# Performance work log

Measured on AMD Instinct MI355X. Metric: run time of the kernel, lower is better.

## Reference

```python
import jax, jax.numpy as jnp
import numpy as np
import math

DIM = 512
WINDOW = 4
TOPK = 8


def setup_inputs() -> dict:
    key = jax.random.key(0)
    ks = jax.random.split(key, 14)
    B, N, D = 4, 4096, DIM
    s = 0.02
    return {
        'mu':  jax.random.normal(ks[0], (B, N, D), jnp.float32),
        'Wq':  jax.random.normal(ks[1], (D, D), jnp.float32) * s,
        'bq':  jnp.zeros((D,), jnp.float32),
        'Wk':  jax.random.normal(ks[2], (D, D), jnp.float32) * s,
        'bk':  jnp.zeros((D,), jnp.float32),
        'Wv':  jax.random.normal(ks[3], (D, D), jnp.float32) * s,
        'bv':  jnp.zeros((D,), jnp.float32),
        'Wm1': jax.random.normal(ks[4], (2 * D, D), jnp.float32) * s,
        'bm1': jnp.zeros((D,), jnp.float32),
        'Wm2': jax.random.normal(ks[5], (D, D), jnp.float32) * s,
        'bm2': jnp.zeros((D,), jnp.float32),
        'Wo':  jax.random.normal(ks[6], (2 * D, D), jnp.float32) * s,
        'bo':  jnp.zeros((D,), jnp.float32),
    }


def reference(mu, Wq, bq, Wk, bk, Wv, bv, Wm1, bm1, Wm2, bm2, Wo, bo):
    B, N, D = mu.shape
    W = WINDOW
    # ---- local windowed message passing ----
    padded = jnp.pad(mu, ((0, 0), (W, 0), (0, 0)))  # left-pad seq with W zeros
    # neighbors[:, n, w-1] = mu[:, n-w] (zeros if n-w < 0); [B, N, W, D]
    neighbors = jnp.stack([padded[:, W - w:W - w + N, :] for w in range(1, W + 1)], axis=2)
    self_exp = jnp.broadcast_to(mu[:, :, None, :], neighbors.shape)
    h = jnp.concatenate([self_exp, neighbors], axis=-1)  # [B, N, W, 2D]
    h = jax.nn.silu(h @ Wm1 + bm1)
    local_msgs = (h @ Wm2 + bm2).mean(axis=2)  # [B, N, D]
    # ---- sparse causal global attention ----
    q = mu @ Wq + bq
    k = mu @ Wk + bk
    v = mu @ Wv + bv
    scores = jnp.einsum('bnd,bmd->bnm', q, k) * (1.0 / math.sqrt(D))
    causal = jnp.tril(jnp.ones((N, N), bool))
    scores = jnp.where(causal, scores, -jnp.inf)
    # top-k then softmax over kept entries == softmax over scatter(-inf elsewhere)
    topk_vals, topk_idx = jax.lax.top_k(scores, TOPK)  # [B, N, K]
    probs = jax.nn.softmax(topk_vals, axis=-1)
    bi = jnp.arange(B)[:, None, None]
    ni = jnp.arange(N)[None, :, None]
    attn = jnp.zeros_like(scores).at[bi, ni, topk_idx].set(probs)  # [B, N, N]
    global_msgs = jnp.einsum('bnm,bmd->bnd', attn, v)
    return jnp.concatenate([local_msgs, global_msgs], axis=-1) @ Wo + bo
```

## Files before the change

kernel.cpp:

```cpp
#include <hip/hip_runtime.h>
#include <math.h>

#define DIM 512
#define NSEQ 4096
#define BATCH 4
#define ROWS (BATCH * NSEQ)

typedef unsigned long long u64;
typedef unsigned int u32;
typedef unsigned short u16;
typedef __attribute__((ext_vector_type(8))) short bf16x8;
typedef __attribute__((ext_vector_type(4))) float f32x4;

typedef const __attribute__((address_space(1))) void* gas1;
typedef __attribute__((address_space(3))) void* las3;

__device__ __forceinline__ u32 to_bf16(float f) {
  u32 x = __float_as_uint(f);
  return (x + 0x7fffu + ((x >> 16) & 1u)) >> 16;
}
__device__ __forceinline__ u32 pk2(float a, float b) {
  return to_bf16(a) | (to_bf16(b) << 16);
}
__device__ __forceinline__ uint4 pk8(float4 a, float4 b) {
  return make_uint4(pk2(a.x, a.y), pk2(a.z, a.w), pk2(b.x, b.y), pk2(b.z, b.w));
}

__device__ __forceinline__ void insert_top8(u64 (&a)[8], u64 key) {
  if (key <= a[7]) return;
  a[7] = key;
#pragma unroll
  for (int i = 7; i > 0; --i) {
    u64 x = a[i - 1], y = a[i];
    u64 hi = x > y ? x : y;
    u64 lo = x > y ? y : x;
    a[i - 1] = hi;
    a[i] = lo;
  }
}
template<int NN>
__device__ __forceinline__ void insert_topN(u64 (&a)[NN], u64 key) {
  if (key <= a[NN - 1]) return;
  a[NN - 1] = key;
#pragma unroll
  for (int i = NN - 1; i > 0; --i) {
    u64 x = a[i - 1], y = a[i];
    u64 hi = x > y ? x : y;
    u64 lo = x > y ? y : x;
    a[i - 1] = hi;
    a[i] = lo;
  }
}
__device__ __forceinline__ float decode_val(u64 key) {
  u32 ord = (u32)(key >> 32);
  u32 s = (ord & 0x80000000u) ? (ord ^ 0x80000000u) : ~ord;
  return __uint_as_float(s);
}
__device__ __forceinline__ u64 pack_key(float v, int m) {
  u32 sb = __float_as_uint(v);
  u32 ord = sb ^ ((sb >> 31) ? 0xFFFFFFFFu : 0x80000000u);
  return ((u64)ord << 32) | (u32)(~(u32)m);
}

__device__ __forceinline__ int fbal(int sub) {
  const int g = sub >> 5, i = sub & 31;
  return (g == 0) ? i : (g == 1) ? (63 - i) : (g == 2) ? (64 + i) : (127 - i);
}

__global__ __launch_bounds__(256) void gemm64qk(const float* __restrict__ mu,
                                                const float* __restrict__ Wq,
                                                const float* __restrict__ bq,
                                                const float* __restrict__ Wk,
                                                const float* __restrict__ bk,
                                                float* __restrict__ Q,
                                                float* __restrict__ Kf,
                                                u16* __restrict__ Kc,
                                                u16* __restrict__ Mu16) {
  __shared__ float As[16][132];
  __shared__ float Bs[16][132];
  const int tid = threadIdx.x;
  const int tx = tid & 15, ty = tid >> 4;
  const int bx = blockIdx.x;
  const bool isK = bx >= 4;
  const int n0 = (bx & 3) * 128;
  const int m0 = blockIdx.y * 128;
  const float* W = isK ? Wk : Wq;
  const float* bias = isK ? bk : bq;
  float* C = isK ? Kf : Q;
  const int arow = tid >> 1, ah8 = (tid & 1) * 8;
  const int bkk = tid >> 4, bc8 = (tid & 15) * 8;
  float acc[8][8] = {};
  for (int k0 = 0; k0 < DIM; k0 += 16) {
    float4 a0 = *(const float4*)(mu + (size_t)(m0 + arow) * DIM + (k0 + ah8));
    float4 a1 = *(const float4*)(mu + (size_t)(m0 + arow) * DIM + (k0 + ah8 + 4));
    float4 b0 = *(const float4*)(W + (size_t)(k0 + bkk) * DIM + (n0 + bc8));
    float4 b1 = *(const float4*)(W + (size_t)(k0 + bkk) * DIM + (n0 + bc8 + 4));
    if (bx == 0)
      *(uint4*)(Mu16 + (size_t)(m0 + arow) * DIM + k0 + ah8) = pk8(a0, a1);
    As[ah8 + 0][arow] = a0.x; As[ah8 + 1][arow] = a0.y;
    As[ah8 + 2][arow] = a0.z; As[ah8 + 3][arow] = a0.w;
    As[ah8 + 4][arow] = a1.x; As[ah8 + 5][arow] = a1.y;
    As[ah8 + 6][arow] = a1.z; As[ah8 + 7][arow] = a1.w;
    *(float4*)&Bs[bkk][bc8] = b0;
    *(float4*)&Bs[bkk][bc8 + 4] = b1;
    __syncthreads();
#pragma unroll
    for (int kk = 0; kk < 16; ++kk) {
      float4 av0 = *(const float4*)&As[kk][ty * 8];
      float4 av1 = *(const float4*)&As[kk][ty * 8 + 4];
      float4 bv0 = *(const float4*)&Bs[kk][tx * 8];
      float4 bv1 = *(const float4*)&Bs[kk][tx * 8 + 4];
      float a8[8] = {av0.x, av0.y, av0.z, av0.w, av1.x, av1.y, av1.z, av1.w};
      float b8[8] = {bv0.x, bv0.y, bv0.z, bv0.w, bv1.x, bv1.y, bv1.z, bv1.w};
#pragma unroll
      for (int i = 0; i < 8; ++i)
#pragma unroll
        for (int j = 0; j < 8; ++j)
          acc[i][j] = fmaf(a8[i], b8[j], acc[i][j]);
    }
    __syncthreads();
  }
  float4 bb0 = *(const float4*)(bias + n0 + tx * 8);
  float4 bb1 = *(const float4*)(bias + n0 + tx * 8 + 4);
#pragma unroll
  for (int i = 0; i < 8; ++i) {
    int row = m0 + ty * 8 + i;
#pragma unroll
    for (int jb = 0; jb < 2; ++jb) {
      int col = n0 + tx * 8 + jb * 4;
      float4 bb = jb ? bb1 : bb0;
      float4 o;
      o.x = acc[i][jb * 4 + 0] + bb.x;
      o.y = acc[i][jb * 4 + 1] + bb.y;
      o.z = acc[i][jb * 4 + 2] + bb.z;
      o.w = acc[i][jb * 4 + 3] + bb.w;
      *(float4*)(C + (size_t)row * DIM + col) = o;
      if (isK) {
        int batch = row >> 12, key = row & 4095;
        int kt = key >> 6, kl = key & 63;
        int chunk = col >> 5;
        size_t didx = ((size_t)batch << 21) +
                      ((size_t)((kt * 16 + chunk) * 64 + kl)) * 32 + (col & 31);
        *(uint2*)(Kc + didx) = make_uint2(pk2(o.x, o.y), pk2(o.z, o.w));
      }
    }
  }
}

__global__ __launch_bounds__(256) void wtrans7(const float* __restrict__ Wv,
                                               const float* __restrict__ Wm1,
                                               const float* __restrict__ Wm2,
                                               const float* __restrict__ Wo,
                                               u16* __restrict__ WT) {
  const size_t DD = (size_t)DIM * DIM;
  const int y = blockIdx.y;
  u16* dst = WT + (size_t)y * DD;
  int o = blockIdx.x * 256 + threadIdx.x;
  if (y == 6) {
    const float* s = Wm2 + (size_t)o * 4;
    ((uint2*)dst)[o] = make_uint2(pk2(s[0], s[1]), pk2(s[2], s[3]));
    return;
  }
  const float* src = (y == 0) ? Wv
                   : (y == 1) ? Wm1
                   : (y == 2) ? Wm1 + DD
                   : (y == 3) ? Wm2
                   : (y == 4) ? Wo
                              : Wo + DD;
  int n = o >> 7;
  int k0 = (o & 127) * 4;
  float a0 = src[(size_t)(k0 + 0) * DIM + n];
  float a1 = src[(size_t)(k0 + 1) * DIM + n];
  float a2 = src[(size_t)(k0 + 2) * DIM + n];
  float a3 = src[(size_t)(k0 + 3) * DIM + n];
  ((uint2*)dst)[(n << 7) + (k0 >> 2)] = make_uint2(pk2(a0, a1), pk2(a2, a3));
}

__global__ __launch_bounds__(256) void wtrans1(const float* __restrict__ src,
                                               u16* __restrict__ dst) {
  int o = blockIdx.x * 256 + threadIdx.x;
  int n = o >> 7;
  int k0 = (o & 127) * 4;
  float a0 = src[(size_t)(k0 + 0) * DIM + n];
  float a1 = src[(size_t)(k0 + 1) * DIM + n];
  float a2 = src[(size_t)(k0 + 2) * DIM + n];
  float a3 = src[(size_t)(k0 + 3) * DIM + n];
  ((uint2*)dst)[(n << 7) + (k0 >> 2)] = make_uint2(pk2(a0, a1), pk2(a2, a3));
}

__global__ void bcomb_k(const float* __restrict__ bm2, const float* __restrict__ Wo,
                        const float* __restrict__ bo, float* __restrict__ bc) {
  int c = blockIdx.x * 256 + threadIdx.x;
  if (c >= DIM) return;
  float s = bo[c];
  for (int k = 0; k < DIM; ++k) s = fmaf(bm2[k], Wo[(size_t)k * DIM + c], s);
  bc[c] = s;
}

__global__ __launch_bounds__(256, 4) void gemmbf(const u16* __restrict__ A, int lda,
                                                 const u16* __restrict__ WT,
                                                 const float* __restrict__ bias,
                                                 float* C, int ldc, int accum) {
  __shared__ u16 As[128 * 32];
  __shared__ u16 Bs[128 * 32];
  const int tid = threadIdx.x;
  const int n0 = blockIdx.x * 128;
  const int m0 = blockIdx.y * 128;
  const int l = tid & 63, lr = l & 15, lu = l >> 4;
  const int wid = tid >> 6, wr = wid >> 1, wc = wid & 1;
  const int lrow = l >> 2, lseg = (l & 3) * 8;
  f32x4 acc[4][4] = {};
  for (int k0 = 0; k0 < 512; k0 += 32) {
    __syncthreads();
#pragma unroll
    for (int j = 0; j < 2; ++j) {
      int r0 = wid * 32 + j * 16;
      const u16* sa = A + (size_t)(m0 + r0 + lrow) * lda + k0 + lseg;
      const u16* sb = WT + (size_t)(n0 + r0 + lrow) * 512 + k0 + lseg;
      __builtin_amdgcn_global_load_lds((gas1)sa, (las3)&As[r0 * 32], 16, 0, 0);
      __builtin_amdgcn_global_load_lds((gas1)sb, (las3)&Bs[r0 * 32], 16, 0, 0);
    }
    __syncthreads();
    bf16x8 af[4], bf_[4];
#pragma unroll
    for (int fr = 0; fr < 4; ++fr) {
      int row = wr * 64 + fr * 16 + lr;
      af[fr] = *(const bf16x8*)&As[row * 32 + lu * 8];
    }
#pragma unroll
    for (int fc = 0; fc < 4; ++fc) {
      int col = wc * 64 + fc * 16 + lr;
      bf_[fc] = *(const bf16x8*)&Bs[col * 32 + lu * 8];
    }
#pragma unroll
    for (int fr = 0; fr < 4; ++fr)
#pragma unroll
      for (int fc = 0; fc < 4; ++fc)
        acc[fr][fc] = __builtin_amdgcn_mfma_f32_16x16x32_bf16(af[fr], bf_[fc], acc[fr][fc], 0, 0, 0);
  }
#pragma unroll
  for (int fr = 0; fr < 4; ++fr)
#pragma unroll
    for (int fc = 0; fc < 4; ++fc) {
      int col = n0 + wc * 64 + fc * 16 + lr;
      float bb = bias ? bias[col] : 0.f;
#pragma unroll
      for (int j = 0; j < 4; ++j) {
        int row = m0 + wr * 64 + fr * 16 + lu * 4 + j;
        size_t off = (size_t)row * ldc + col;
        float o = acc[fr][fc][j] + bb;
        if (accum) o += C[off];
        C[off] = o;
      }
    }
}

__global__ __launch_bounds__(256) void silu_combine(const float* P,
                                                    const float* bm1,
                                                    u16* Gout16) {
  size_t idx = (size_t)blockIdx.x * 256 + threadIdx.x;
  int r = (int)(idx >> 7);
  int c4 = (int)(idx & 127);
  int n = r & (NSEQ - 1);
  const float4* P4 = (const float4*)P;
  float4 a = P4[(size_t)r * 256 + c4];
  float4 bm = ((const float4*)bm1)[c4];
  float bx = a.x + bm.x, by = a.y + bm.y, bz = a.z + bm.z, bw = a.w + bm.w;
  float sx = 0.f, sy = 0.f, sz = 0.f, sw = 0.f;
#pragma unroll
  for (int w = 1; w <= 4; ++w) {
    float ex = bx, ey = by, ez = bz, ew = bw;
    if (n >= w) {
      float4 nb = P4[(size_t)(r - w) * 256 + 128 + c4];
      ex += nb.x; ey += nb.y; ez += nb.z; ew += nb.w;
    }
    sx += ex / (1.f + expf(-ex));
    sy += ey / (1.f + expf(-ey));
    sz += ez / (1.f + expf(-ez));
    sw += ew / (1.f + expf(-ew));
  }
  *(uint2*)(Gout16 + (size_t)r * 512 + c4 * 4) =
      make_uint2(pk2(0.25f * sx, 0.25f * sy), pk2(0.25f * sz, 0.25f * sw));
}

__global__ __launch_bounds__(256, 4) void attn_fused(const float* __restrict__ Qf,
                                                     const float* __restrict__ Kf,
                                                     const u16* __restrict__ Kc,
                                                     const float* __restrict__ V,
                                                     u16* __restrict__ G) {
  __shared__ union UA {
    struct { u16 Qs[16 * 512]; u64 cand[256][8]; } s;
    float Qf32[16][512];
  } uA;
  __shared__ int cidx[16][16];
  __shared__ u64 exkey[16][16];
  __shared__ float psm[16][8];
  __shared__ int pidx[16][8];

  const int tid = threadIdx.x;
  const int bid = blockIdx.x;
  const int xcd = bid & 7;
  const int b = xcd >> 1;
  const int par = xcd & 1;
  const int sub = bid >> 3;
  const int qt = 2 * fbal(sub) + par;
  const int n0 = qt * 16;
  const size_t rb = (size_t)b * NSEQ;
  const float SCALE_F = 0.04419417382415922f;

  const int l = tid & 63, lr = l & 15, lu = l >> 4;
  const int wid = tid >> 6;
  const int mbase = lu * 4;

  {
    int row = tid >> 4, part = tid & 15;
    const float4* src = (const float4*)(Qf + ((rb + n0 + row) << 9));
#pragma unroll
    for (int c = 0; c < 4; ++c) {
      int slot = part * 4 + c;
      float4 x = src[slot * 2], y = src[slot * 2 + 1];
      *(uint4*)&uA.s.Qs[row * 512 + (slot ^ (row & 7)) * 8] = pk8(x, y);
    }
  }
  __syncthreads();

  u64 best[8] = {};
  const int nq = n0 + lr;

  const int nkt = (n0 + 16 + 63) >> 6;
  const int lo = (lr * 32) + lu * 8;
  for (int kt = wid; kt < nkt; kt += 4) {
    const int m0 = kt << 6;
    const u16* kb = Kc + ((size_t)b << 21) + (size_t)kt * 32768;
    f32x4 acc[4] = {};
    bf16x8 kcur[4], knxt[4];
#pragma unroll
    for (int fk = 0; fk < 4; ++fk)
      kcur[fk] = *(const bf16x8*)(kb + fk * 512 + lo);
#pragma unroll
    for (int ks = 0; ks < 16; ++ks) {
      if (ks < 15) {
        const u16* cb = kb + (ks + 1) * 2048;
#pragma unroll
        for (int fk = 0; fk < 4; ++fk)
          knxt[fk] = *(const bf16x8*)(cb + fk * 512 + lo);
      }
      bf16x8 qf = *(const bf16x8*)&uA.s.Qs[lr * 512 + ((ks * 4 + lu) ^ (lr & 7)) * 8];
#pragma unroll
      for (int fk = 0; fk < 4; ++fk)
        acc[fk] = __builtin_amdgcn_mfma_f32_16x16x32_bf16(kcur[fk], qf, acc[fk], 0, 0, 0);
      if (ks < 15) {
#pragma unroll
        for (int fk = 0; fk < 4; ++fk) kcur[fk] = knxt[fk];
      }
    }
    if (m0 + 63 <= n0) {
#pragma unroll
      for (int fk = 0; fk < 4; ++fk)
#pragma unroll
        for (int j = 0; j < 4; ++j)
          insert_top8(best, pack_key(acc[fk][j], m0 + fk * 16 + mbase + j));
    } else {
#pragma unroll
      for (int fk = 0; fk < 4; ++fk)
#pragma unroll
        for (int j = 0; j < 4; ++j) {
          int m = m0 + fk * 16 + mbase + j;
          if (m <= nq) insert_top8(best, pack_key(acc[fk][j], m));
        }
    }
  }

  __syncthreads();
#pragma unroll
  for (int i = 0; i < 8; ++i) uA.s.cand[tid][i] = best[i];
  __syncthreads();

  if (tid < 16) {
    u64 mb[16] = {};
    for (int w = 0; w < 4; ++w)
      for (int u = 0; u < 4; ++u) {
        const u64* cl = uA.s.cand[w * 64 + u * 16 + tid];
#pragma unroll
        for (int i = 0; i < 8; ++i) insert_topN<16>(mb, cl[i]);
      }
#pragma unroll
    for (int i = 0; i < 16; ++i)
      cidx[tid][i] = (mb[i] != 0ULL) ? (int)(~(u32)mb[i]) : -1;
  }
  __syncthreads();

  {
    int row = tid >> 4, seg = tid & 15;
    const float4* src = (const float4*)(Qf + ((rb + n0 + row) << 9));
    float4* dst = (float4*)&uA.Qf32[row][0];
#pragma unroll
    for (int c = 0; c < 8; ++c) dst[seg * 8 + c] = src[seg * 8 + c];
  }
  __syncthreads();

  {
    const int g = tid >> 2;
    const int lsub = tid & 3;
    const int qi = g >> 2;
    const int cblk = g & 3;
    const float4* q4 = (const float4*)&uA.Qf32[qi][0];
#pragma unroll
    for (int cc = 0; cc < 4; ++cc) {
      int c = cblk * 4 + cc;
      int ci = cidx[qi][c];
      float4 p = make_float4(0.f, 0.f, 0.f, 0.f);
      if (ci >= 0) {
        const float4* k4 = (const float4*)(Kf + ((rb + ci) << 9));
#pragma unroll 8
        for (int t = 0; t < 32; ++t) {
          float4 kv = k4[4 * t + lsub];
          float4 qv = q4[4 * t + lsub];
          p.x = fmaf(kv.x, qv.x, p.x);
          p.y = fmaf(kv.y, qv.y, p.y);
          p.z = fmaf(kv.z, qv.z, p.z);
          p.w = fmaf(kv.w, qv.w, p.w);
        }
      }
      p.x += __shfl_xor(p.x, 2);
      p.y += __shfl_xor(p.y, 2);
      p.z += __shfl_xor(p.z, 2);
      p.w += __shfl_xor(p.w, 2);
      p.x += __shfl_xor(p.x, 1);
      p.y += __shfl_xor(p.y, 1);
      p.z += __shfl_xor(p.z, 1);
      p.w += __shfl_xor(p.w, 1);
      float rx = p.x + p.z;
      float ry = p.y + p.w;
      float r = rx + ry;
      if (lsub == 0)
        exkey[qi][c] = (ci >= 0) ? pack_key(r * SCALE_F, ci) : 0ULL;
    }
  }
  __syncthreads();

  if (tid < 16) {
    u64 mb[8] = {};
#pragma unroll
    for (int t2 = 0; t2 < 16; ++t2) insert_top8(mb, exkey[tid][t2]);
    float vmax = decode_val(mb[0]);
    float e[8];
#pragma unroll
    for (int i = 0; i < 8; ++i)
      e[i] = (mb[i] != 0ULL) ? expf(decode_val(mb[i]) - vmax) : 0.f;
    float s01 = e[0] + e[1], s23 = e[2] + e[3];
    float s45 = e[4] + e[5], s67 = e[6] + e[7];
    float ssum = (s01 + s23) + (s45 + s67);
#pragma unroll
    for (int i = 0; i < 8; ++i) {
      psm[tid][i] = e[i] / ssum;
      pidx[tid][i] = (mb[i] != 0ULL) ? (int)(~(u32)mb[i]) : 0;
    }
  }
  __syncthreads();

  {
    const int qi = tid >> 4, seg = tid & 15;
    float pp[8];
    int ix[8];
#pragma unroll
    for (int i = 0; i < 8; ++i) { pp[i] = psm[qi][i]; ix[i] = pidx[qi][i]; }
    const float4* V4 = (const float4*)V;
    u16* Gb = G + ((size_t)(rb + n0 + qi)) * 512 + seg * 32;
#pragma unroll
    for (int it = 0; it < 8; ++it) {
      float4 a = make_float4(0.f, 0.f, 0.f, 0.f);
#pragma unroll
      for (int i = 0; i < 8; ++i) {
        float4 vv = V4[((rb + ix[i]) << 7) + seg * 8 + it];
        a.x = fmaf(pp[i], vv.x, a.x);
        a.y = fmaf(pp[i], vv.y, a.y);
        a.z = fmaf(pp[i], vv.z, a.z);
        a.w = fmaf(pp[i], vv.w, a.w);
      }
      *(uint2*)(Gb + it * 4) = make_uint2(pk2(a.x, a.y), pk2(a.z, a.w));
    }
  }
}

extern "C" void kernel_launch(void* const* d_in, const int* in_sizes, int n_in,
                              void* d_out, int out_size, void* d_ws, size_t ws_size,
                              hipStream_t stream) {
  const float* mu = (const float*)d_in[0];
  const float* Wq = (const float*)d_in[1];
  const float* bq = (const float*)d_in[2];
  const float* Wk = (const float*)d_in[3];
  const float* bk = (const float*)d_in[4];
  const float* Wv = (const float*)d_in[5];
  const float* bv = (const float*)d_in[6];
  const float* Wm1 = (const float*)d_in[7];
  const float* bm1 = (const float*)d_in[8];
  const float* Wm2 = (const float*)d_in[9];
  const float* bm2 = (const float*)d_in[10];
  const float* Wo = (const float*)d_in[11];
  const float* bo = (const float*)d_in[12];
  float* out = (float*)d_out;

  float* ws = (float*)d_ws;
  const size_t RD = (size_t)ROWS * DIM;
  const size_t DD = (size_t)DIM * DIM;
  float* X1 = ws;
  float* X2 = X1 + RD;
  float* X3 = X2 + RD;
  float* X4 = X3 + RD;
  u16* Kc = (u16*)(X4 + RD);
  u16* WT = Kc + RD;
  u16* WvT = WT;
  u16* Wm1aT = WT + DD;
  u16* WoTT = WT + 4 * DD;
  u16* WoBT = WT + 5 * DD;
  u16* Wm216 = WT + 6 * DD;
  float* Wcombf = (float*)(WT + 7 * DD);
  u16* WcombT = (u16*)(Wcombf + DD);
  float* bcomb = (float*)(WcombT + DD);
  u16* Mu16 = (u16*)(bcomb + 512);

  dim3 blk(256);
  dim3 gqk(8, ROWS / 128);
  dim3 gbf(DIM / 128, ROWS / 128);
  dim3 gbf2(2 * DIM / 128, ROWS / 128);

  wtrans7<<<dim3(256, 7), blk, 0, stream>>>(Wv, Wm1, Wm2, Wo, WT);

  gemmbf<<<dim3(4, 4), blk, 0, stream>>>(Wm216, 512, WoTT, (const float*)nullptr, Wcombf, 512, 0);
  bcomb_k<<<dim3(2), blk, 0, stream>>>(bm2, Wo, bo, bcomb);
  wtrans1<<<dim3(256), blk, 0, stream>>>(Wcombf, WcombT);

  gemm64qk<<<gqk, blk, 0, stream>>>(mu, Wq, bq, Wk, bk, X1, X2, Kc, Mu16);

  gemmbf<<<gbf, blk, 0, stream>>>(Mu16, 512, WvT, bv, X3, 512, 0);

  attn_fused<<<dim3(1024), blk, 0, stream>>>(X1, X2, Kc, X3, (u16*)X4);

  gemmbf<<<gbf2, blk, 0, stream>>>(Mu16, 512, Wm1aT, (const float*)nullptr, X1, 1024, 0);
  silu_combine<<<dim3(ROWS * 128 / 256), blk, 0, stream>>>(X1, bm1, (u16*)X3);

  gemmbf<<<gbf, blk, 0, stream>>>((u16*)X3, 512, WcombT, bcomb, out, 512, 0);
  gemmbf<<<gbf, blk, 0, stream>>>((u16*)X4, 512, WoBT, (const float*)nullptr, out, 512, 1);
}
```

Baseline: 697.4 us.

## Merge projection GEMMs and attention/SiLU stages into role-split mega kernels

The Q/K fp32 GEMM, V GEMM and Wm1 GEMM become one launch (mega1) whose blocks pick a role from their index. The V and Wm1 GEMMs now read fp32 mu, convert it to bf16 into a swizzled LDS tile, and write bf16 outputs. Attention and the SiLU neighbour combine share a second launch (mega2), with V and the Wm1 products read as bf16. The two final output GEMMs become one K=1024 GEMM over a concatenated activation and a concatenated weight, which drops the accumulate pass over the output. This removes launches, the separate Mu16 staging, fp32 intermediate traffic and one full output read-modify-write. In exchange, intermediates are stored at lower precision, and mixing heterogeneous roles in one grid can cause load imbalance and occupancy limits set by the largest role's LDS.

```diff
diff --git a/kernel.cpp b/kernel.cpp
--- a/kernel.cpp
+++ b/kernel.cpp
@@ -24,6 +24,9 @@
 }
 __device__ __forceinline__ uint4 pk8(float4 a, float4 b) {
   return make_uint4(pk2(a.x, a.y), pk2(a.z, a.w), pk2(b.x, b.y), pk2(b.z, b.w));
+}
+__device__ __forceinline__ float bf2f(u32 lo16) {
+  return __uint_as_float(lo16 << 16);
 }
 
 __device__ __forceinline__ void insert_top8(u64 (&a)[8], u64 key) {
@@ -67,23 +70,133 @@
   return (g == 0) ? i : (g == 1) ? (63 - i) : (g == 2) ? (64 + i) : (127 - i);
 }
 
-__global__ __launch_bounds__(256) void gemm64qk(const float* __restrict__ mu,
-                                                const float* __restrict__ Wq,
-                                                const float* __restrict__ bq,
-                                                const float* __restrict__ Wk,
-                                                const float* __restrict__ bk,
-                                                float* __restrict__ Q,
-                                                float* __restrict__ Kf,
-                                                u16* __restrict__ Kc,
-                                                u16* __restrict__ Mu16) {
-  __shared__ float As[16][132];
-  __shared__ float Bs[16][132];
+__global__ __launch_bounds__(256) void wtrans7(const float* __restrict__ Wv,
+                                               const float* __restrict__ Wm1,
+                                               const float* __restrict__ Wm2,
+                                               const float* __restrict__ Wo,
+                                               u16* __restrict__ WT) {
+  const size_t DD = (size_t)DIM * DIM;
+  const int y = blockIdx.y;
+  u16* dst = WT + (size_t)y * DD;
+  int o = blockIdx.x * 256 + threadIdx.x;
+  if (y == 6) {
+    const float* s = Wm2 + (size_t)o * 4;
+    ((uint2*)dst)[o] = make_uint2(pk2(s[0], s[1]), pk2(s[2], s[3]));
+    return;
+  }
+  const float* src = (y == 0) ? Wv
+                   : (y == 1) ? Wm1
+                   : (y == 2) ? Wm1 + DD
+                   : (y == 3) ? Wm2
+                   : (y == 4) ? Wo
+                              : Wo + DD;
+  int n = o >> 7;
+  int k0 = (o & 127) * 4;
+  float a0 = src[(size_t)(k0 + 0) * DIM + n];
+  float a1 = src[(size_t)(k0 + 1) * DIM + n];
+  float a2 = src[(size_t)(k0 + 2) * DIM + n];
+  float a3 = src[(size_t)(k0 + 3) * DIM + n];
+  ((uint2*)dst)[(n << 7) + (k0 >> 2)] = make_uint2(pk2(a0, a1), pk2(a2, a3));
+}
+
+__global__ __launch_bounds__(256) void wtrans2(const float* __restrict__ Wcombf,
+                                               const u16* __restrict__ WoBT,
+                                               u16* __restrict__ WT2) {
+  int o = blockIdx.x * 256 + threadIdx.x;
+  int n = o >> 8;
+  int k = (o & 255) * 4;
+  if (k < 512) {
+    float a0 = Wcombf[(size_t)(k + 0) * DIM + n];
+    float a1 = Wcombf[(size_t)(k + 1) * DIM + n];
+    float a2 = Wcombf[(size_t)(k + 2) * DIM + n];
+    float a3 = Wcombf[(size_t)(k + 3) * DIM + n];
+    *(uint2*)&WT2[(size_t)n * 1024 + k] = make_uint2(pk2(a0, a1), pk2(a2, a3));
+  } else {
+    *(uint2*)&WT2[(size_t)n * 1024 + k] = *(const uint2*)&WoBT[(size_t)n * 512 + (k - 512)];
+  }
+}
+
+__global__ void bcomb_k(const float* __restrict__ bm2, const float* __restrict__ Wo,
+                        const float* __restrict__ bo, float* __restrict__ bc) {
+  int c = blockIdx.x * 256 + threadIdx.x;
+  if (c >= DIM) return;
+  float s = bo[c];
+  for (int k = 0; k < DIM; ++k) s = fmaf(bm2[k], Wo[(size_t)k * DIM + c], s);
+  bc[c] = s;
+}
+
+__global__ __launch_bounds__(256, 4) void gemmbf(const u16* __restrict__ A, int lda,
+                                                 const u16* __restrict__ WT, int K,
+                                                 const float* __restrict__ bias,
+                                                 float* C, int ldc) {
+  __shared__ u16 As[128 * 32];
+  __shared__ u16 Bs[128 * 32];
+  const int tid = threadIdx.x;
+  const int n0 = blockIdx.x * 128;
+  const int m0 = blockIdx.y * 128;
+  const int l = tid & 63, lr = l & 15, lu = l >> 4;
+  const int wid = tid >> 6, wr = wid >> 1, wc = wid & 1;
+  const int lrow = l >> 2, lseg = (l & 3) * 8;
+  f32x4 acc[4][4] = {};
+  for (int k0 = 0; k0 < K; k0 += 32) {
+    __syncthreads();
+#pragma unroll
+    for (int j = 0; j < 2; ++j) {
+      int r0 = wid * 32 + j * 16;
+      const u16* sa = A + (size_t)(m0 + r0 + lrow) * lda + k0 + lseg;
+      const u16* sb = WT + (size_t)(n0 + r0 + lrow) * K + k0 + lseg;
+      __builtin_amdgcn_global_load_lds((gas1)sa, (las3)&As[r0 * 32], 16, 0, 0);
+      __builtin_amdgcn_global_load_lds((gas1)sb, (las3)&Bs[r0 * 32], 16, 0, 0);
+    }
+    __syncthreads();
+    bf16x8 af[4], bf_[4];
+#pragma unroll
+    for (int fr = 0; fr < 4; ++fr) {
+      int row = wr * 64 + fr * 16 + lr;
+      af[fr] = *(const bf16x8*)&As[row * 32 + lu * 8];
+    }
+#pragma unroll
+    for (int fc = 0; fc < 4; ++fc) {
+      int col = wc * 64 + fc * 16 + lr;
+      bf_[fc] = *(const bf16x8*)&Bs[col * 32 + lu * 8];
+    }
+#pragma unroll
+    for (int fr = 0; fr < 4; ++fr)
+#pragma unroll
+      for (int fc = 0; fc < 4; ++fc)
+        acc[fr][fc] = __builtin_amdgcn_mfma_f32_16x16x32_bf16(af[fr], bf_[fc], acc[fr][fc], 0, 0, 0);
+  }
+#pragma unroll
+  for (int fr = 0; fr < 4; ++fr)
+#pragma unroll
+    for (int fc = 0; fc < 4; ++fc) {
+      int col = n0 + wc * 64 + fc * 16 + lr;
+      float bb = bias ? bias[col] : 0.f;
+#pragma unroll
+      for (int j = 0; j < 4; ++j) {
+        int row = m0 + wr * 64 + fr * 16 + lu * 4 + j;
+        C[(size_t)row * ldc + col] = acc[fr][fc][j] + bb;
+      }
+    }
+}
+
+union M1LDS {
+  struct { float As[16][132]; float Bs[16][132]; } q;
+  struct { u16 As[128 * 32]; u16 Bs[128 * 32]; } g;
+};
+
+__device__ void qk_body(int idx, M1LDS& sh,
+                        const float* mu, const float* Wq, const float* bq,
+                        const float* Wk, const float* bk,
+                        float* Q, float* Kf, u16* Kc) {
+  float (&As)[16][132] = sh.q.As;
+  float (&Bs)[16][132] = sh.q.Bs;
   const int tid = threadIdx.x;
   const int tx = tid & 15, ty = tid >> 4;
-  const int bx = blockIdx.x;
+  const int bx = idx & 7;
   const bool isK = bx >= 4;
   const int n0 = (bx & 3) * 128;
-  const int m0 = blockIdx.y * 128;
+  const int m0 = (idx >> 3) * 128;
   const float* W = isK ? Wk : Wq;
   const float* bias = isK ? bk : bq;
   float* C = isK ? Kf : Q;
@@ -95,8 +208,6 @@
     float4 a1 = *(const float4*)(mu + (size_t)(m0 + arow) * DIM + (k0 + ah8 + 4));
     float4 b0 = *(const float4*)(W + (size_t)(k0 + bkk) * DIM + (n0 + bc8));
     float4 b1 = *(const float4*)(W + (size_t)(k0 + bkk) * DIM + (n0 + bc8 + 4));
-    if (bx == 0)
-      *(uint4*)(Mu16 + (size_t)(m0 + arow) * DIM + k0 + ah8) = pk8(a0, a1);
     As[ah8 + 0][arow] = a0.x; As[ah8 + 1][arow] = a0.y;
     As[ah8 + 2][arow] = a0.z; As[ah8 + 3][arow] = a0.w;
     As[ah8 + 4][arow] = a1.x; As[ah8 + 5][arow] = a1.y;
@@ -147,77 +258,30 @@
   }
 }
 
-__global__ __launch_bounds__(256) void wtrans7(const float* __restrict__ Wv,
-                                               const float* __restrict__ Wm1,
-                                               const float* __restrict__ Wm2,
-                                               const float* __restrict__ Wo,
-                                               u16* __restrict__ WT) {
-  const size_t DD = (size_t)DIM * DIM;
-  const int y = blockIdx.y;
-  u16* dst = WT + (size_t)y * DD;
-  int o = blockIdx.x * 256 + threadIdx.x;
-  if (y == 6) {
-    const float* s = Wm2 + (size_t)o * 4;
-    ((uint2*)dst)[o] = make_uint2(pk2(s[0], s[1]), pk2(s[2], s[3]));
-    return;
-  }
-  const float* src = (y == 0) ? Wv
-                   : (y == 1) ? Wm1
-                   : (y == 2) ? Wm1 + DD
-                   : (y == 3) ? Wm2
-                   : (y == 4) ? Wo
-                              : Wo + DD;
-  int n = o >> 7;
-  int k0 = (o & 127) * 4;
-  float a0 = src[(size_t)(k0 + 0) * DIM + n];
-  float a1 = src[(size_t)(k0 + 1) * DIM + n];
-  float a2 = src[(size_t)(k0 + 2) * DIM + n];
-  float a3 = src[(size_t)(k0 + 3) * DIM + n];
-  ((uint2*)dst)[(n << 7) + (k0 >> 2)] = make_uint2(pk2(a0, a1), pk2(a2, a3));
-}
-
-__global__ __launch_bounds__(256) void wtrans1(const float* __restrict__ src,
-                                               u16* __restrict__ dst) {
-  int o = blockIdx.x * 256 + threadIdx.x;
-  int n = o >> 7;
-  int k0 = (o & 127) * 4;
-  float a0 = src[(size_t)(k0 + 0) * DIM + n];
-  float a1 = src[(size_t)(k0 + 1) * DIM + n];
-  float a2 = src[(size_t)(k0 + 2) * DIM + n];
-  float a3 = src[(size_t)(k0 + 3) * DIM + n];
-  ((uint2*)dst)[(n << 7) + (k0 >> 2)] = make_uint2(pk2(a0, a1), pk2(a2, a3));
-}
-
-__global__ void bcomb_k(const float* __restrict__ bm2, const float* __restrict__ Wo,
-                        const float* __restrict__ bo, float* __restrict__ bc) {
-  int c = blockIdx.x * 256 + threadIdx.x;
-  if (c >= DIM) return;
-  float s = bo[c];
-  for (int k = 0; k < DIM; ++k) s = fmaf(bm2[k], Wo[(size_t)k * DIM + c], s);
-  bc[c] = s;
-}
-
-__global__ __launch_bounds__(256, 4) void gemmbf(const u16* __restrict__ A, int lda,
-                                                 const u16* __restrict__ WT,
-                                                 const float* __restrict__ bias,
-                                                 float* C, int ldc, int accum) {
-  __shared__ u16 As[128 * 32];
-  __shared__ u16 Bs[128 * 32];
+__device__ void gemm_f32A(int n0, int m0, M1LDS& sh,
+                          const float* A, const u16* WT,
+                          const float* bias, u16* Cb, int ldc) {
+  u16* As = sh.g.As;
+  u16* Bs = sh.g.Bs;
   const int tid = threadIdx.x;
-  const int n0 = blockIdx.x * 128;
-  const int m0 = blockIdx.y * 128;
   const int l = tid & 63, lr = l & 15, lu = l >> 4;
   const int wid = tid >> 6, wr = wid >> 1, wc = wid & 1;
   const int lrow = l >> 2, lseg = (l & 3) * 8;
+  const int srow = tid >> 1, shalf = tid & 1;
   f32x4 acc[4][4] = {};
   for (int k0 = 0; k0 < 512; k0 += 32) {
     __syncthreads();
+    {
+      const float4* a4 = (const float4*)(A + (size_t)(m0 + srow) * 512 + k0 + shalf * 16);
+      float4 u0 = a4[0], u1 = a4[1], u2 = a4[2], u3 = a4[3];
+      int sw = (srow >> 1) & 3;
+      *(uint4*)&As[srow * 32 + ((shalf * 2 + 0) ^ sw) * 8] = pk8(u0, u1);
+      *(uint4*)&As[srow * 32 + ((shalf * 2 + 1) ^ sw) * 8] = pk8(u2, u3);
+    }
 #pragma unroll
     for (int j = 0; j < 2; ++j) {
       int r0 = wid * 32 + j * 16;
-      const u16* sa = A + (size_t)(m0 + r0 + lrow) * lda + k0 + lseg;
       const u16* sb = WT + (size_t)(n0 + r0 + lrow) * 512 + k0 + lseg;
-      __builtin_amdgcn_global_load_lds((gas1)sa, (las3)&As[r0 * 32], 16, 0, 0);
       __builtin_amdgcn_global_load_lds((gas1)sb, (las3)&Bs[r0 * 32], 16, 0, 0);
     }
     __syncthreads();
@@ -225,7 +289,7 @@
 #pragma unroll
     for (int fr = 0; fr < 4; ++fr) {
       int row = wr * 64 + fr * 16 + lr;
-      af[fr] = *(const bf16x8*)&As[row * 32 + lu * 8];
+      af[fr] = *(const bf16x8*)&As[row * 32 + (lu ^ ((row >> 1) & 3)) * 8];
     }
 #pragma unroll
     for (int fc = 0; fc < 4; ++fc) {
@@ -247,58 +311,49 @@
 #pragma unroll
       for (int j = 0; j < 4; ++j) {
         int row = m0 + wr * 64 + fr * 16 + lu * 4 + j;
-        size_t off = (size_t)row * ldc + col;
-        float o = acc[fr][fc][j] + bb;
-        if (accum) o += C[off];
-        C[off] = o;
-      }
-    }
-}
-
-__global__ __launch_bounds__(256) void silu_combine(const float* P,
-                                                    const float* bm1,
-                                                    u16* Gout16) {
-  size_t idx = (size_t)blockIdx.x * 256 + threadIdx.x;
-  int r = (int)(idx >> 7);
-  int c4 = (int)(idx & 127);
-  int n = r & (NSEQ - 1);
-  const float4* P4 = (const float4*)P;
-  float4 a = P4[(size_t)r * 256 + c4];
-  float4 bm = ((const float4*)bm1)[c4];
-  float bx = a.x + bm.x, by = a.y + bm.y, bz = a.z + bm.z, bw = a.w + bm.w;
-  float sx = 0.f, sy = 0.f, sz = 0.f, sw = 0.f;
-#pragma unroll
-  for (int w = 1; w <= 4; ++w) {
-    float ex = bx, ey = by, ez = bz, ew = bw;
-    if (n >= w) {
-      float4 nb = P4[(size_t)(r - w) * 256 + 128 + c4];
-      ex += nb.x; ey += nb.y; ez += nb.z; ew += nb.w;
-    }
-    sx += ex / (1.f + expf(-ex));
-    sy += ey / (1.f + expf(-ey));
-    sz += ez / (1.f + expf(-ez));
-    sw += ew / (1.f + expf(-ew));
-  }
-  *(uint2*)(Gout16 + (size_t)r * 512 + c4 * 4) =
-      make_uint2(pk2(0.25f * sx, 0.25f * sy), pk2(0.25f * sz, 0.25f * sw));
-}
-
-__global__ __launch_bounds__(256, 4) void attn_fused(const float* __restrict__ Qf,
-                                                     const float* __restrict__ Kf,
-                                                     const u16* __restrict__ Kc,
-                                                     const float* __restrict__ V,
-                                                     u16* __restrict__ G) {
-  __shared__ union UA {
-    struct { u16 Qs[16 * 512]; u64 cand[256][8]; } s;
-    float Qf32[16][512];
-  } uA;
-  __shared__ int cidx[16][16];
-  __shared__ u64 exkey[16][16];
-  __shared__ float psm[16][8];
-  __shared__ int pidx[16][8];
-
+        Cb[(size_t)row * ldc + col] = (u16)to_bf16(acc[fr][fc][j] + bb);
+      }
+    }
+}
+
+__global__ __launch_bounds__(256) void mega1(const float* __restrict__ mu,
+                                             const float* __restrict__ Wq,
+                                             const float* __restrict__ bq,
+                                             const float* __restrict__ Wk,
+                                             const float* __restrict__ bk,
+                                             const u16* __restrict__ WvT,
+                                             const float* __restrict__ bv,
+                                             const u16* __restrict__ Wm1aT,
+                                             float* __restrict__ Q,
+                                             float* __restrict__ Kf,
+                                             u16* __restrict__ Kc,
+                                             u16* __restrict__ V16,
+                                             u16* __restrict__ Pair) {
+  __shared__ M1LDS sh;
+  const int bid = blockIdx.x;
+  const int role = bid % 5;
+  const int grp = bid / 5;
+  if (role < 2) {
+    qk_body(grp * 2 + role, sh, mu, Wq, bq, Wk, bk, Q, Kf, Kc);
+  } else if (role == 2) {
+    gemm_f32A((grp & 3) * 128, (grp >> 2) * 128, sh, mu, WvT, bv, V16, 512);
+  } else {
+    int i = grp * 2 + (role - 3);
+    gemm_f32A((i & 7) * 128, (i >> 3) * 128, sh, mu, Wm1aT, nullptr, Pair, 1024);
+  }
+}
+
+union UA {
+  struct { u16 Qs[16 * 512]; u64 cand[256][8]; } s;
+  float Qf32[16][512];
+};
+
+__device__ void attn_body(int bid, UA& uA,
+                          const float* Qf, const float* Kf, const u16* Kc,
+                          const u16* V16, u16* P16,
+                          int (&cidx)[16][16], u64 (&exkey)[16][16],
+                          float (&psm)[16][8], int (&pidx)[16][8]) {
   const int tid = threadIdx.x;
-  const int bid = blockIdx.x;
   const int xcd = bid & 7;
   const int b = xcd >> 1;
   const int par = xcd & 1;
@@ -465,21 +520,76 @@
     int ix[8];
 #pragma unroll
     for (int i = 0; i < 8; ++i) { pp[i] = psm[qi][i]; ix[i] = pidx[qi][i]; }
-    const float4* V4 = (const float4*)V;
-    u16* Gb = G + ((size_t)(rb + n0 + qi)) * 512 + seg * 32;
+    u16* Gb = P16 + ((size_t)(rb + n0 + qi)) * 1024 + 512 + seg * 32;
 #pragma unroll
     for (int it = 0; it < 8; ++it) {
       float4 a = make_float4(0.f, 0.f, 0.f, 0.f);
 #pragma unroll
       for (int i = 0; i < 8; ++i) {
-        float4 vv = V4[((rb + ix[i]) << 7) + seg * 8 + it];
-        a.x = fmaf(pp[i], vv.x, a.x);
-        a.y = fmaf(pp[i], vv.y, a.y);
-        a.z = fmaf(pp[i], vv.z, a.z);
-        a.w = fmaf(pp[i], vv.w, a.w);
+        uint2 vv = *(const uint2*)(V16 + ((size_t)(rb + ix[i])) * 512 + seg * 32 + it * 4);
+        a.x = fmaf(pp[i], bf2f(vv.x & 0xffffu), a.x);
+        a.y = fmaf(pp[i], __uint_as_float(vv.x & 0xffff0000u), a.y);
+        a.z = fmaf(pp[i], bf2f(vv.y & 0xffffu), a.z);
+        a.w = fmaf(pp[i], __uint_as_float(vv.y & 0xffff0000u), a.w);
       }
       *(uint2*)(Gb + it * 4) = make_uint2(pk2(a.x, a.y), pk2(a.z, a.w));
     }
+  }
+}
+
+__device__ void silu_body(int sidx, const u16* Pair, const float* bm1, u16* P16) {
+#pragma unroll
+  for (int t = 0; t < 4; ++t) {
+    size_t idx = (size_t)sidx * 1024 + t * 256 + threadIdx.x;
+    int r = (int)(idx >> 7);
+    int c4 = (int)(idx & 127);
+    int n = r & (NSEQ - 1);
+    uint2 av = *(const uint2*)&Pair[(size_t)r * 1024 + c4 * 4];
+    const float4 bm = ((const float4*)bm1)[c4];
+    float bx = bf2f(av.x & 0xffffu) + bm.x;
+    float by = __uint_as_float(av.x & 0xffff0000u) + bm.y;
+    float bz = bf2f(av.y & 0xffffu) + bm.z;
+    float bw = __uint_as_float(av.y & 0xffff0000u) + bm.w;
+    float sx = 0.f, sy = 0.f, sz = 0.f, sw = 0.f;
+#pragma unroll
+    for (int w = 1; w <= 4; ++w) {
+      float ex = bx, ey = by, ez = bz, ew = bw;
+      if (n >= w) {
+        uint2 nb = *(const uint2*)&Pair[(size_t)(r - w) * 1024 + 512 + c4 * 4];
+        ex += bf2f(nb.x & 0xffffu);
+        ey += __uint_as_float(nb.x & 0xffff0000u);
+        ez += bf2f(nb.y & 0xffffu);
+        ew += __uint_as_float(nb.y & 0xffff0000u);
+      }
+      sx += ex / (1.f + expf(-ex));
+      sy += ey / (1.f + expf(-ey));
+      sz += ez / (1.f + expf(-ez));
+      sw += ew / (1.f + expf(-ew));
+    }
+    *(uint2*)&P16[(size_t)r * 1024 + c4 * 4] =
+        make_uint2(pk2(0.25f * sx, 0.25f * sy), pk2(0.25f * sz, 0.25f * sw));
+  }
+}
+
+__global__ __launch_bounds__(256, 4) void mega2(const float* __restrict__ Qf,
+                                                const float* __restrict__ Kf,
+                                                const u16* __restrict__ Kc,
+                                                const u16* __restrict__ V16,
+                                                const u16* __restrict__ Pair,
+                                                const float* __restrict__ bm1,
+                                                u16* __restrict__ P16) {
+  __shared__ UA uA;
+  __shared__ int cidx[16][16];
+  __shared__ u64 exkey[16][16];
+  __shared__ float psm[16][8];
+  __shared__ int pidx[16][8];
+  const int bid = blockIdx.x;
+  const int role = bid % 3;
+  const int grp = bid / 3;
+  if (role == 0) {
+    attn_body(grp, uA, Qf, Kf, Kc, V16, P16, cidx, exkey, psm, pidx);
+  } else {
+    silu_body(grp * 2 + (role - 1), Pair, bm1, P16);
   }
 }
 
@@ -506,40 +616,31 @@
   const size_t DD = (size_t)DIM * DIM;
   float* X1 = ws;
   float* X2 = X1 + RD;
-  float* X3 = X2 + RD;
-  float* X4 = X3 + RD;
-  u16* Kc = (u16*)(X4 + RD);
-  u16* WT = Kc + RD;
+  u16* Pair = (u16*)(X2 + RD);
+  u16* P16 = Pair + RD * 2;
+  u16* Kc = P16 + RD * 2;
+  u16* V16 = Kc + RD;
+  u16* WT = V16 + RD;
   u16* WvT = WT;
   u16* Wm1aT = WT + DD;
   u16* WoTT = WT + 4 * DD;
   u16* WoBT = WT + 5 * DD;
   u16* Wm216 = WT + 6 * DD;
-  float* Wcombf = (float*)(WT + 7 * DD);
-  u16* WcombT = (u16*)(Wcombf + DD);
-  float* bcomb = (float*)(WcombT + DD);
-  u16* Mu16 = (u16*)(bcomb + 512);
+  u16* WT2 = WT + 7 * DD;
+  float* Wcombf = (float*)(WT2 + (size_t)512 * 1024);
+  float* bcomb = Wcombf + DD;
 
   dim3 blk(256);
-  dim3 gqk(8, ROWS / 128);
-  dim3 gbf(DIM / 128, ROWS / 128);
-  dim3 gbf2(2 * DIM / 128, ROWS / 128);
 
   wtrans7<<<dim3(256, 7), blk, 0, stream>>>(Wv, Wm1, Wm2, Wo, WT);
-
-  gemmbf<<<dim3(4, 4), blk, 0, stream>>>(Wm216, 512, WoTT, (const float*)nullptr, Wcombf, 512, 0);
+  gemmbf<<<dim3(4, 4), blk, 0, stream>>>(Wm216, 512, WoTT, 512, (const float*)nullptr, Wcombf, 512);
   bcomb_k<<<dim3(2), blk, 0, stream>>>(bm2, Wo, bo, bcomb);
-  wtrans1<<<dim3(256), blk, 0, stream>>>(Wcombf, WcombT);
-
-  gemm64qk<<<gqk, blk, 0, stream>>>(mu, Wq, bq, Wk, bk, X1, X2, Kc, Mu16);
-
-  gemmbf<<<gbf, blk, 0, stream>>>(Mu16, 512, WvT, bv, X3, 512, 0);
-
-  attn_fused<<<dim3(1024), blk, 0, stream>>>(X1, X2, Kc, X3, (u16*)X4);
-
-  gemmbf<<<gbf2, blk, 0, stream>>>(Mu16, 512, Wm1aT, (const float*)nullptr, X1, 1024, 0);
-  silu_combine<<<dim3(ROWS * 128 / 256), blk, 0, stream>>>(X1, bm1, (u16*)X3);
-
-  gemmbf<<<gbf, blk, 0, stream>>>((u16*)X3, 512, WcombT, bcomb, out, 512, 0);
-  gemmbf<<<gbf, blk, 0, stream>>>((u16*)X4, 512, WoBT, (const float*)nullptr, out, 512, 1);
-}
+  wtrans2<<<dim3(512), blk, 0, stream>>>(Wcombf, WoBT, WT2);
+
+  mega1<<<dim3(2560), blk, 0, stream>>>(mu, Wq, bq, Wk, bk, WvT, bv, Wm1aT,
+                                        X1, X2, Kc, V16, Pair);
+
+  mega2<<<dim3(3072), blk, 0, stream>>>(X1, X2, Kc, V16, Pair, bm1, P16);
+
+  gemmbf<<<dim3(4, 128), blk, 0, stream>>>(P16, 1024, WT2, 1024, bcomb, out, 512);
+}
```

After: 875.6 us. 1.26x slower.

## Concatenate local and global messages into one K=1024 output GEMM

Applied to the files above, without the earlier changes.

Attention and silu_combine now write their bf16 outputs into the two halves of a single [rows,1024] buffer. The two final output GEMMs, one of which re-read and accumulated into out, become one GEMM with K=1024 against a concatenated transposed weight built by a new wtrans2 kernel. This removes one launch and the fp32 read-modify-write of the output. It also adds s_setprio around the MFMA block in the attention score loop.

```diff
diff --git a/kernel.cpp b/kernel.cpp
--- a/kernel.cpp
+++ b/kernel.cpp
@@ -176,16 +176,21 @@
   ((uint2*)dst)[(n << 7) + (k0 >> 2)] = make_uint2(pk2(a0, a1), pk2(a2, a3));
 }
 
-__global__ __launch_bounds__(256) void wtrans1(const float* __restrict__ src,
-                                               u16* __restrict__ dst) {
+__global__ __launch_bounds__(256) void wtrans2(const float* __restrict__ Wcombf,
+                                               const u16* __restrict__ WoBT,
+                                               u16* __restrict__ WT2) {
   int o = blockIdx.x * 256 + threadIdx.x;
-  int n = o >> 7;
-  int k0 = (o & 127) * 4;
-  float a0 = src[(size_t)(k0 + 0) * DIM + n];
-  float a1 = src[(size_t)(k0 + 1) * DIM + n];
-  float a2 = src[(size_t)(k0 + 2) * DIM + n];
-  float a3 = src[(size_t)(k0 + 3) * DIM + n];
-  ((uint2*)dst)[(n << 7) + (k0 >> 2)] = make_uint2(pk2(a0, a1), pk2(a2, a3));
+  int n = o >> 8;
+  int k = (o & 255) * 4;
+  if (k < 512) {
+    float a0 = Wcombf[(size_t)(k + 0) * DIM + n];
+    float a1 = Wcombf[(size_t)(k + 1) * DIM + n];
+    float a2 = Wcombf[(size_t)(k + 2) * DIM + n];
+    float a3 = Wcombf[(size_t)(k + 3) * DIM + n];
+    *(uint2*)&WT2[(size_t)n * 1024 + k] = make_uint2(pk2(a0, a1), pk2(a2, a3));
+  } else {
+    *(uint2*)&WT2[(size_t)n * 1024 + k] = *(const uint2*)&WoBT[(size_t)n * 512 + (k - 512)];
+  }
 }
 
 __global__ void bcomb_k(const float* __restrict__ bm2, const float* __restrict__ Wo,
@@ -198,9 +203,9 @@
 }
 
 __global__ __launch_bounds__(256, 4) void gemmbf(const u16* __restrict__ A, int lda,
-                                                 const u16* __restrict__ WT,
+                                                 const u16* __restrict__ WT, int K,
                                                  const float* __restrict__ bias,
-                                                 float* C, int ldc, int accum) {
+                                                 float* C, int ldc) {
   __shared__ u16 As[128 * 32];
   __shared__ u16 Bs[128 * 32];
   const int tid = threadIdx.x;
@@ -210,13 +215,13 @@
   const int wid = tid >> 6, wr = wid >> 1, wc = wid & 1;
   const int lrow = l >> 2, lseg = (l & 3) * 8;
   f32x4 acc[4][4] = {};
-  for (int k0 = 0; k0 < 512; k0 += 32) {
+  for (int k0 = 0; k0 < K; k0 += 32) {
     __syncthreads();
 #pragma unroll
     for (int j = 0; j < 2; ++j) {
       int r0 = wid * 32 + j * 16;
       const u16* sa = A + (size_t)(m0 + r0 + lrow) * lda + k0 + lseg;
-      const u16* sb = WT + (size_t)(n0 + r0 + lrow) * 512 + k0 + lseg;
+      const u16* sb = WT + (size_t)(n0 + r0 + lrow) * K + k0 + lseg;
       __builtin_amdgcn_global_load_lds((gas1)sa, (las3)&As[r0 * 32], 16, 0, 0);
       __builtin_amdgcn_global_load_lds((gas1)sb, (las3)&Bs[r0 * 32], 16, 0, 0);
     }
@@ -247,17 +252,14 @@
 #pragma unroll
       for (int j = 0; j < 4; ++j) {
         int row = m0 + wr * 64 + fr * 16 + lu * 4 + j;
-        size_t off = (size_t)row * ldc + col;
-        float o = acc[fr][fc][j] + bb;
-        if (accum) o += C[off];
-        C[off] = o;
+        C[(size_t)row * ldc + col] = acc[fr][fc][j] + bb;
       }
     }
 }
 
 __global__ __launch_bounds__(256) void silu_combine(const float* P,
                                                     const float* bm1,
-                                                    u16* Gout16) {
+                                                    u16* P16) {
   size_t idx = (size_t)blockIdx.x * 256 + threadIdx.x;
   int r = (int)(idx >> 7);
   int c4 = (int)(idx & 127);
@@ -279,7 +281,7 @@
     sz += ez / (1.f + expf(-ez));
     sw += ew / (1.f + expf(-ew));
   }
-  *(uint2*)(Gout16 + (size_t)r * 512 + c4 * 4) =
+  *(uint2*)(P16 + (size_t)r * 1024 + c4 * 4) =
       make_uint2(pk2(0.25f * sx, 0.25f * sy), pk2(0.25f * sz, 0.25f * sw));
 }
 
@@ -287,7 +289,7 @@
                                                      const float* __restrict__ Kf,
                                                      const u16* __restrict__ Kc,
                                                      const float* __restrict__ V,
-                                                     u16* __restrict__ G) {
+                                                     u16* __restrict__ P16) {
   __shared__ union UA {
     struct { u16 Qs[16 * 512]; u64 cand[256][8]; } s;
     float Qf32[16][512];
@@ -346,9 +348,11 @@
           knxt[fk] = *(const bf16x8*)(cb + fk * 512 + lo);
       }
       bf16x8 qf = *(const bf16x8*)&uA.s.Qs[lr * 512 + ((ks * 4 + lu) ^ (lr & 7)) * 8];
+      __builtin_amdgcn_s_setprio(1);
 #pragma unroll
       for (int fk = 0; fk < 4; ++fk)
         acc[fk] = __builtin_amdgcn_mfma_f32_16x16x32_bf16(kcur[fk], qf, acc[fk], 0, 0, 0);
+      __builtin_amdgcn_s_setprio(0);
       if (ks < 15) {
 #pragma unroll
         for (int fk = 0; fk < 4; ++fk) kcur[fk] = knxt[fk];
@@ -466,7 +470,7 @@
 #pragma unroll
     for (int i = 0; i < 8; ++i) { pp[i] = psm[qi][i]; ix[i] = pidx[qi][i]; }
     const float4* V4 = (const float4*)V;
-    u16* Gb = G + ((size_t)(rb + n0 + qi)) * 512 + seg * 32;
+    u16* Gb = P16 + ((size_t)(rb + n0 + qi)) * 1024 + 512 + seg * 32;
 #pragma unroll
     for (int it = 0; it < 8; ++it) {
       float4 a = make_float4(0.f, 0.f, 0.f, 0.f);
@@ -507,17 +511,17 @@
   float* X1 = ws;
   float* X2 = X1 + RD;
   float* X3 = X2 + RD;
-  float* X4 = X3 + RD;
-  u16* Kc = (u16*)(X4 + RD);
+  u16* P16 = (u16*)(X3 + RD);
+  u16* Kc = P16 + RD * 2;
   u16* WT = Kc + RD;
   u16* WvT = WT;
   u16* Wm1aT = WT + DD;
   u16* WoTT = WT + 4 * DD;
   u16* WoBT = WT + 5 * DD;
   u16* Wm216 = WT + 6 * DD;
-  float* Wcombf = (float*)(WT + 7 * DD);
-  u16* WcombT = (u16*)(Wcombf + DD);
-  float* bcomb = (float*)(WcombT + DD);
+  u16* WT2 = WT + 7 * DD;
+  float* Wcombf = (float*)(WT2 + (size_t)512 * 1024);
+  float* bcomb = Wcombf + DD;
   u16* Mu16 = (u16*)(bcomb + 512);
 
   dim3 blk(256);
@@ -526,20 +530,18 @@
   dim3 gbf2(2 * DIM / 128, ROWS / 128);
 
   wtrans7<<<dim3(256, 7), blk, 0, stream>>>(Wv, Wm1, Wm2, Wo, WT);
-
-  gemmbf<<<dim3(4, 4), blk, 0, stream>>>(Wm216, 512, WoTT, (const float*)nullptr, Wcombf, 512, 0);
+  gemmbf<<<dim3(4, 4), blk, 0, stream>>>(Wm216, 512, WoTT, 512, (const float*)nullptr, Wcombf, 512);
   bcomb_k<<<dim3(2), blk, 0, stream>>>(bm2, Wo, bo, bcomb);
-  wtrans1<<<dim3(256), blk, 0, stream>>>(Wcombf, WcombT);
+  wtrans2<<<dim3(512), blk, 0, stream>>>(Wcombf, WoBT, WT2);
 
   gemm64qk<<<gqk, blk, 0, stream>>>(mu, Wq, bq, Wk, bk, X1, X2, Kc, Mu16);
 
-  gemmbf<<<gbf, blk, 0, stream>>>(Mu16, 512, WvT, bv, X3, 512, 0);
-
-  attn_fused<<<dim3(1024), blk, 0, stream>>>(X1, X2, Kc, X3, (u16*)X4);
-
-  gemmbf<<<gbf2, blk, 0, stream>>>(Mu16, 512, Wm1aT, (const float*)nullptr, X1, 1024, 0);
-  silu_combine<<<dim3(ROWS * 128 / 256), blk, 0, stream>>>(X1, bm1, (u16*)X3);
-
-  gemmbf<<<gbf, blk, 0, stream>>>((u16*)X3, 512, WcombT, bcomb, out, 512, 0);
-  gemmbf<<<gbf, blk, 0, stream>>>((u16*)X4, 512, WoBT, (const float*)nullptr, out, 512, 1);
-}
+  gemmbf<<<gbf, blk, 0, stream>>>(Mu16, 512, WvT, 512, bv, X3, 512);
+
+  attn_fused<<<dim3(1024), blk, 0, stream>>>(X1, X2, Kc, X3, P16);
+
+  gemmbf<<<gbf2, blk, 0, stream>>>(Mu16, 512, Wm1aT, 512, (const float*)nullptr, X1, 1024);
+  silu_combine<<<dim3(ROWS * 128 / 256), blk, 0, stream>>>(X1, bm1, P16);
+
+  gemmbf<<<dim3(4, 128), blk, 0, stream>>>(P16, 1024, WT2, 1024, bcomb, out, 512);
+}
```

Result: faster. 655.5 us (-6.0%).
